# Kernel optimization log

Hardware: AMD Instinct MI355X
Metric: run time of the kernel (lower is better)

Reference implementation:

```python
import jax, jax.numpy as jnp
import numpy as np

H, D, CR, SEL_K = 8, 64, 32, 16          # query heads, head dim, block size, top-k blocks
ROPE_DIM, THETA, WINDOW, GROUPS = 32, 10000.0, 512, 2
INTER, HID, QC = 512, 1024, 256
NEG = -1e30


def _rope_cache(t):
    half = ROPE_DIM // 2
    inv = 1.0 / (THETA ** (jnp.arange(half, dtype=jnp.float32) * 2.0 / ROPE_DIM))
    ang = jnp.arange(t, dtype=jnp.float32)[:, None] * inv[None, :]  # (t, half)
    return jnp.cos(ang), jnp.sin(ang)


def _apply_partial_rope(x, cos, sin):
    half = ROPE_DIM // 2
    x1, x2, rest = x[..., :half], x[..., half:ROPE_DIM], x[..., ROPE_DIM:]
    return jnp.concatenate([x1 * cos - x2 * sin, x1 * sin + x2 * cos, rest], -1)


def _rmsnorm(x, g, eps=1e-6):
    return x * jax.lax.rsqrt(jnp.mean(x * x, -1, keepdims=True) + eps) * g


def setup_inputs():
    key = jax.random.key(0)
    ks = jax.random.split(key, 9)
    f = lambda k, shp, s: jax.random.normal(k, shp, jnp.float32) * s
    return {
        "h": f(ks[0], (1, 2048, HID), 1.0),
        "w_qc": f(ks[1], (HID, QC), QC ** -0.5),
        "w_qup": f(ks[2], (QC, H * D), (H * D) ** -0.5),
        "w_k": f(ks[3], (HID, D), HID ** -0.5),
        "w_v": f(ks[4], (HID, D), HID ** -0.5),
        "g_qnorm": jnp.ones((D,), jnp.float32),
        "g_knorm": jnp.ones((D,), jnp.float32),
        "w_gate": f(ks[5], (D, 3), 0.05),
        "b_gate": jnp.zeros((3,), jnp.float32),
        "sink_logit": f(ks[6], (H,), 0.1),
        "w_out_group": f(ks[7], (GROUPS, (H // GROUPS) * D, INTER), 0.05),
        "w_out": f(ks[8], (GROUPS * INTER, HID), 0.03),
    }


def reference(h, w_qc, w_qup, w_k, w_v, g_qnorm, g_knorm, w_gate, b_gate,
              sink_logit, w_out_group, w_out):
    b, t, _ = h.shape
    cos, sin = _rope_cache(t)
    q = (h @ w_qc @ w_qup).reshape(b, t, H, D).transpose(0, 2, 1, 3)  # (b,H,t,D)
    q = _rmsnorm(_apply_partial_rope(q, cos, sin), g_qnorm)
    k = _rmsnorm(_apply_partial_rope(h @ w_k, cos, sin), g_knorm)      # (b,t,D)
    v = h @ w_v                                                        # (b,t,D)
    scale = 1.0 / np.sqrt(D).astype(np.float32)
    qpos = jnp.arange(t)
    sink = jnp.broadcast_to(sink_logit[None, :, None, None], (b, H, t, 1))

    # ---- compressed branch: attend over block-mean pooled K/V ----
    nb = t // CR
    kc = k[:, :nb * CR].reshape(b, nb, CR, D).mean(2)                  # (b,nb,D)
    vc = v[:, :nb * CR].reshape(b, nb, CR, D).mean(2)
    comp_valid = ((jnp.arange(nb) + 1) * CR - 1)[None, :] <= qpos[:, None]  # (t,nb)
    any_blk = comp_valid.any(-1, keepdims=True)                        # (t,1)
    safe = jnp.where(any_blk, comp_valid, True)
    sc_raw = jnp.einsum('bhqd,bnd->bhqn', q, kc) * scale
    pc = jax.nn.softmax(jnp.concatenate([jnp.where(safe, sc_raw, NEG), sink], -1), -1)
    comp_out = jnp.einsum('bhqn,bnd->bhqd', pc[..., :nb], vc)
    comp_out = jnp.where(any_blk[None, None], comp_out, 0.0)

    # ---- selective branch: top-k blocks per query, dense-masked gather-equivalent ----
    sel_sc = jnp.where(comp_valid, sc_raw, -jnp.inf)
    top_idx = jax.lax.top_k(sel_sc, min(SEL_K, nb))[1]                 # (b,H,t,K)
    sel_blocks = (top_idx[..., :, None] == jnp.arange(nb)).any(-2)     # (b,H,t,nb)
    block_of = jnp.minimum(qpos // CR, nb - 1)
    causal = qpos[:, None] >= qpos[None, :]                            # (t,t)
    in_range = qpos < nb * CR
    tok_sel = sel_blocks[..., block_of] & (causal & in_range[None, :])[None, None]
    scores_full = jnp.einsum('bhqd,bkd->bhqk', q, k) * scale           # (b,H,t,t)
    ps = jax.nn.softmax(jnp.where(tok_sel, scores_full, NEG), -1)
    sel_out = jnp.einsum('bhqk,bkd->bhqd', ps, v)

    # ---- sliding-window branch ----
    sw = causal & ((qpos[:, None] - qpos[None, :]) < WINDOW)
    pw = jax.nn.softmax(
        jnp.concatenate([jnp.where(sw[None, None], scores_full, NEG), sink], -1), -1)
    sw_out = jnp.einsum('bhqk,bkd->bhqd', pw[..., :t], v)

    # ---- learned gate over the three branches ----
    g = jax.nn.sigmoid(q @ w_gate + b_gate)                            # (b,H,t,3)
    g = g / jnp.clip(g.sum(-1, keepdims=True), 1e-6)
    mixed = g[..., 0:1] * comp_out + g[..., 1:2] * sel_out + g[..., 2:3] * sw_out

    # ---- grouped output projection ----
    x = mixed.transpose(0, 2, 1, 3).reshape(b, t, GROUPS, (H // GROUPS) * D)
    y = jnp.einsum('btgf,gfi->btgi', x, w_out_group).reshape(b, t, GROUPS * INTER)
    return y @ w_out
```

## Files before the change

kernel.cpp:

```cpp
#include <hip/hip_runtime.h>
#include <hip/hip_bf16.h>
#include <float.h>
#include <math.h>

typedef __hip_bfloat16 bf16;
typedef float v2f __attribute__((ext_vector_type(2)));

#define NEGBIG (-1e30f)

__device__ __forceinline__ float ldv(const float* p, int i) { return p[i]; }

__device__ __forceinline__ float wave_sum(float v) {
#pragma unroll
  for (int off = 32; off; off >>= 1) v += __shfl_xor(v, off, 64);
  return v;
}
__device__ __forceinline__ float wave_max(float v) {
#pragma unroll
  for (int off = 32; off; off >>= 1) v = fmaxf(v, __shfl_xor(v, off, 64));
  return v;
}

__device__ __forceinline__ float rdlane(float v, int l) {
  return __uint_as_float(__builtin_amdgcn_readlane(__float_as_uint(v), l));
}

template <int L0>
__device__ __forceinline__ void pv16(const float* __restrict__ vp, float e,
                                     float& a0, float& a1, float& a2, float& a3) {
#pragma unroll
  for (int t = 0; t < 16; t += 4) {
    float p0 = rdlane(e, L0 + t + 0);
    float p1 = rdlane(e, L0 + t + 1);
    float p2 = rdlane(e, L0 + t + 2);
    float p3 = rdlane(e, L0 + t + 3);
    a0 += p0 * vp[(t + 0) * 64];
    a1 += p1 * vp[(t + 1) * 64];
    a2 += p2 * vp[(t + 2) * 64];
    a3 += p3 * vp[(t + 3) * 64];
  }
}

__device__ __forceinline__ float qk_dot(const float4* __restrict__ qr,
                                        const float4* __restrict__ kp) {
  v2f d01 = {0.f, 0.f}, d23 = {0.f, 0.f};
#pragma unroll 1
  for (int i = 0; i < 16; i += 2) {
    float4 q0 = qr[i],     k0 = kp[i * 32];
    float4 q1 = qr[i + 1], k1 = kp[i * 32 + 32];
    d01 += (v2f){q0.x, q0.y} * (v2f){k0.x, k0.y};
    d23 += (v2f){q0.z, q0.w} * (v2f){k0.z, k0.w};
    d01 += (v2f){q1.x, q1.y} * (v2f){k1.x, k1.y};
    d23 += (v2f){q1.z, q1.w} * (v2f){k1.z, k1.w};
  }
  v2f d = d01 + d23;
  return d.x + d.y;
}

__device__ __forceinline__ void gemm_core(
    const float* __restrict__ A, const float* __restrict__ B, float* __restrict__ C,
    int K, int lda, int ldb, int ldc, int row0, int col0)
{
  __shared__ __align__(16) float As[2][16][68];
  __shared__ __align__(16) float Bs[2][16][68];
  const int tid = threadIdx.x;
  const int tx = tid & 15, ty = tid >> 4;
  const int ar = tid >> 2;
  const int ak = (tid & 3) * 4;
  const int bk = tid >> 4;
  const int bc = (tid & 15) * 4;

  const int nk = K >> 4;
  float4 a4 = *reinterpret_cast<const float4*>(&A[(row0 + ar) * lda + ak]);
  float4 b4 = *reinterpret_cast<const float4*>(&B[bk * ldb + col0 + bc]);
  {
    As[0][ak + 0][ar] = a4.x; As[0][ak + 1][ar] = a4.y;
    As[0][ak + 2][ar] = a4.z; As[0][ak + 3][ar] = a4.w;
    *reinterpret_cast<float4*>(&Bs[0][bk][bc]) = b4;
  }

  v2f acc01[4] = {};
  v2f acc23[4] = {};
  for (int t = 0; t < nk; ++t) {
    const int cur = t & 1;
    if (t + 1 < nk) {
      int k0 = (t + 1) * 16;
      a4 = *reinterpret_cast<const float4*>(&A[(row0 + ar) * lda + k0 + ak]);
      b4 = *reinterpret_cast<const float4*>(&B[(k0 + bk) * ldb + col0 + bc]);
    }
    __syncthreads();
#pragma unroll
    for (int kk = 0; kk < 16; ++kk) {
      float4 av = *reinterpret_cast<const float4*>(&As[cur][kk][ty * 4]);
      float4 bv = *reinterpret_cast<const float4*>(&Bs[cur][kk][tx * 4]);
      v2f b01; b01.x = bv.x; b01.y = bv.y;
      v2f b23; b23.x = bv.z; b23.y = bv.w;
      float a[4] = {av.x, av.y, av.z, av.w};
#pragma unroll
      for (int i = 0; i < 4; ++i) {
        v2f as; as.x = a[i]; as.y = a[i];
        acc01[i] += as * b01;
        acc23[i] += as * b23;
      }
    }
    if (t + 1 < nk) {
      const int nxt = cur ^ 1;
      As[nxt][ak + 0][ar] = a4.x; As[nxt][ak + 1][ar] = a4.y;
      As[nxt][ak + 2][ar] = a4.z; As[nxt][ak + 3][ar] = a4.w;
      *reinterpret_cast<float4*>(&Bs[nxt][bk][bc]) = b4;
    }
  }
#pragma unroll
  for (int i = 0; i < 4; ++i) {
    float4 o = make_float4(acc01[i].x, acc01[i].y, acc23[i].x, acc23[i].y);
    *reinterpret_cast<float4*>(&C[(row0 + ty * 4 + i) * ldc + col0 + tx * 4]) = o;
  }
}

__global__ __launch_bounds__(256) void gemm_tile(
    const float* __restrict__ A, const float* __restrict__ B, float* __restrict__ C,
    int M, int N, int K, int lda, int ldb, int ldc)
{
  gemm_core(A, B, C, K, lda, ldb, ldc, blockIdx.y * 64, blockIdx.x * 64);
}

__global__ __launch_bounds__(256) void gemm_kv(
    const float* __restrict__ A, const float* __restrict__ B0, const float* __restrict__ B1,
    float* __restrict__ C0, float* __restrict__ C1, int K, int lda, int ldb, int ldc)
{
  const float* B = blockIdx.x ? B1 : B0;
  float* C = blockIdx.x ? C1 : C0;
  gemm_core(A, B, C, K, lda, ldb, ldc, blockIdx.y * 64, 0);
}

__global__ __launch_bounds__(256) void gemm_dual(
    const float* __restrict__ A0, const float* __restrict__ A1,
    const float* __restrict__ B0, const float* __restrict__ B1,
    float* __restrict__ C0, float* __restrict__ C1,
    int K, int lda, int ldb, int ldc, int nx)
{
  const bool second = (int)blockIdx.x >= nx;
  const float* A = second ? A1 : A0;
  const float* B = second ? B1 : B0;
  float* C = second ? C1 : C0;
  const int bx = second ? (blockIdx.x - nx) : blockIdx.x;
  gemm_core(A, B, C, K, lda, ldb, ldc, blockIdx.y * 64, bx * 64);
}

__global__ __launch_bounds__(256) void rope_table_kernel(float* __restrict__ ct,
                                                         float* __restrict__ st) {
  int tid = blockIdx.x * 256 + threadIdx.x;
  if (tid >= 2048 * 16) return;
  int pos = tid >> 4, i = tid & 15;
  double ang = (double)pos * pow(10000.0, -(double)i / 16.0);
  ct[tid] = (float)cos(ang);
  st[tid] = (float)sin(ang);
}

__global__ __launch_bounds__(256) void rope_rms_kernel(
    float* __restrict__ x, const float* __restrict__ g, int rows, int posShift,
    float* __restrict__ kS, const float* __restrict__ ct, const float* __restrict__ st)
{
  const int lane = threadIdx.x & 63;
  const int wid = threadIdx.x >> 6;
  const int r = blockIdx.x * 4 + wid;
  if (r >= rows) return;
  const int pos = r >> posShift;
  float val = x[r * 64 + lane];
  float p = __shfl_xor(val, 16, 64);
  float out = val;
  if (lane < 32) {
    int i = lane & 15;
    float cc = ct[pos * 16 + i], ss = st[pos * 16 + i];
    out = (lane < 16) ? (val * cc - p * ss) : (p * ss + val * cc);
  }
  float ms = wave_sum(out * out) * (1.0f / 64.0f);
  float rn = rsqrtf(ms + 1e-6f);
  float res = out * rn * ldv(g, lane);
  x[r * 64 + lane] = res;
  if (kS) {
    int f4 = (r >> 5) * 512 + (lane >> 2) * 32 + (r & 31);
    kS[f4 * 4 + (lane & 3)] = res;
  }
}

__global__ void compress_kernel(const float* __restrict__ k, const float* __restrict__ v,
                                float* __restrict__ kcT4, float* __restrict__ vc)
{
  const int n = blockIdx.x;
  const int d = threadIdx.x;
  float sk = 0.f, sv = 0.f;
  for (int j = 0; j < 32; ++j) {
    sk += k[(n * 32 + j) * 64 + d];
    sv += v[(n * 32 + j) * 64 + d];
  }
  kcT4[(d >> 2) * 256 + n * 4 + (d & 3)] = sk * (1.0f / 32.0f);
  vc[n * 64 + d] = sv * (1.0f / 32.0f);
}

__global__ __launch_bounds__(256) void attn_kernel(
    const float* __restrict__ q, const float* __restrict__ kS, const float* __restrict__ vbuf,
    const float* __restrict__ kcT4, const float* __restrict__ vc,
    const float* __restrict__ w_gate, const float* __restrict__ b_gate,
    const float* __restrict__ sink, float* __restrict__ mixed)
{
  __shared__ __align__(16) float shq[4][64];
  __shared__ int shsel[4][16];
  const int lane = threadIdx.x & 63;
  const int wid = threadIdx.x >> 6;
  const int bid = 4095 - blockIdx.x;
  const int r = bid * 4 + wid;
  const int qpos = r >> 3, h = r & 7;
  const float scale = 0.125f;

  float qv = q[r * 64 + lane];
  shq[wid][lane] = qv;

  float z0 = qv * ldv(w_gate, lane * 3 + 0);
  float z1 = qv * ldv(w_gate, lane * 3 + 1);
  float z2 = qv * ldv(w_gate, lane * 3 + 2);
  z0 = wave_sum(z0) + ldv(b_gate, 0);
  z1 = wave_sum(z1) + ldv(b_gate, 1);
  z2 = wave_sum(z2) + ldv(b_gate, 2);
  float ga0 = 1.f / (1.f + expf(-z0));
  float ga1 = 1.f / (1.f + expf(-z1));
  float ga2 = 1.f / (1.f + expf(-z2));
  float gs = fmaxf(ga0 + ga1 + ga2, 1e-6f);
  float ginv = 1.f / gs;
  ga0 *= ginv; ga1 *= ginv; ga2 *= ginv;

  const float4* qr = reinterpret_cast<const float4*>(&shq[wid][0]);
  const float4* ks4 = reinterpret_cast<const float4*>(kS);
  const float4* kct = reinterpret_cast<const float4*>(kcT4);
  const float snk = ldv(sink, h);
  const int nv = (qpos + 1) >> 5;

  float sc;
  {
    float d0 = 0.f, d1 = 0.f;
#pragma unroll 1
    for (int i = 0; i < 16; i += 2) {
      float4 q0 = qr[i],     k0 = kct[i * 64 + lane];
      float4 q1 = qr[i + 1], k1 = kct[(i + 1) * 64 + lane];
      d0 += q0.x * k0.x + q0.z * k0.z;
      d1 += q0.y * k0.y + q0.w * k0.w;
      d0 += q1.x * k1.x + q1.z * k1.z;
      d1 += q1.y * k1.y + q1.w * k1.w;
    }
    sc = (d0 + d1) * scale;
  }

  float comp_out = 0.f;
  if (nv > 0) {
    float scomp = (lane < nv) ? sc : NEGBIG;
    float m = fmaxf(wave_max(scomp), snk);
    float e = (lane < nv) ? expf(sc - m) : 0.f;
    float S = wave_sum(e) + expf(snk - m);
    float pn = e / S;
    const float* vcp = vc + lane;
    float c0 = 0.f, c1 = 0.f, c2 = 0.f, c3 = 0.f;
    pv16<0>(vcp, pn, c0, c1, c2, c3);
    pv16<16>(vcp + 1024, pn, c0, c1, c2, c3);
    pv16<32>(vcp + 2048, pn, c0, c1, c2, c3);
    pv16<48>(vcp + 3072, pn, c0, c1, c2, c3);
    comp_out = (c0 + c1) + (c2 + c3);
  }

  {
    float selv = (lane < nv) ? sc : -FLT_MAX;
#pragma unroll
    for (int it = 0; it < 16; ++it) {
      float bv = selv; int bi = lane;
#pragma unroll
      for (int off = 32; off; off >>= 1) {
        float ov = __shfl_xor(bv, off, 64);
        int oi = __shfl_xor(bi, off, 64);
        if (ov > bv || (ov == bv && oi < bi)) { bv = ov; bi = oi; }
      }
      if (lane == 0) shsel[wid][it] = bi;
      if (lane == bi) selv = -INFINITY;
    }
  }

  float M = NEGBIG, S = 0.f, osel = 0.f;
#pragma unroll 1
  for (int c = 0; c < 8; ++c) {
    int b0 = shsel[wid][2 * c], b1 = shsel[wid][2 * c + 1];
    int base0 = b0 * 32, base1 = b1 * 32;
    if (base0 > qpos && base1 > qpos) continue;
    int myb = (lane < 32) ? b0 : b1;
    int tok = myb * 32 + (lane & 31);
    bool ok = (tok <= qpos);
    const float4* kp = ks4 + myb * 512 + (lane & 31);
    float s = ok ? qk_dot(qr, kp) * scale : NEGBIG;
    float Mn = fmaxf(M, wave_max(s));
    float e = ok ? expf(s - Mn) : 0.f;
    float cs = wave_sum(e);
    float corr = expf(M - Mn);
    S = S * corr + cs;
    const float* v0 = vbuf + base0 * 64 + lane;
    const float* v1 = vbuf + base1 * 64 + lane;
    float a0 = 0.f, a1 = 0.f, a2 = 0.f, a3 = 0.f;
    pv16<0>(v0, e, a0, a1, a2, a3);
    pv16<16>(v0 + 1024, e, a0, a1, a2, a3);
    pv16<32>(v1, e, a0, a1, a2, a3);
    pv16<48>(v1 + 1024, e, a0, a1, a2, a3);
    osel = osel * corr + ((a0 + a1) + (a2 + a3));
    M = Mn;
  }
  osel /= S;

  float Mw = NEGBIG, Sw = 0.f, osw = 0.f;
  int kstart = qpos - 511; if (kstart < 0) kstart = 0;
  int sbf = kstart >> 5, sbl = qpos >> 5;
#pragma unroll 1
  for (int sb = sbf; sb <= sbl; sb += 2) {
    int sb1 = sb + 1;
    bool v1ok = (sb1 <= sbl);
    int sb1c = v1ok ? sb1 : sb;
    int myb = (lane < 32) ? sb : sb1c;
    int tok = myb * 32 + (lane & 31);
    bool ok = (tok >= kstart) && (tok <= qpos) && ((lane < 32) || v1ok);
    const float4* kp = ks4 + myb * 512 + (lane & 31);
    float s = ok ? qk_dot(qr, kp) * scale : NEGBIG;
    float Mn = fmaxf(Mw, wave_max(s));
    float e = ok ? expf(s - Mn) : 0.f;
    float cs = wave_sum(e);
    float corr = expf(Mw - Mn);
    Sw = Sw * corr + cs;
    const float* v0 = vbuf + sb * 2048 + lane;
    const float* v1 = vbuf + sb1c * 2048 + lane;
    float a0 = 0.f, a1 = 0.f, a2 = 0.f, a3 = 0.f;
    pv16<0>(v0, e, a0, a1, a2, a3);
    pv16<16>(v0 + 1024, e, a0, a1, a2, a3);
    pv16<32>(v1, e, a0, a1, a2, a3);
    pv16<48>(v1 + 1024, e, a0, a1, a2, a3);
    osw = osw * corr + ((a0 + a1) + (a2 + a3));
    Mw = Mn;
  }
  {
    float Mf = fmaxf(Mw, snk);
    float corr = expf(Mw - Mf);
    float Sf = Sw * corr + expf(snk - Mf);
    osw = osw * corr / Sf;
  }

  mixed[r * 64 + lane] = ga0 * comp_out + ga1 * osel + ga2 * osw;
}

extern "C" void kernel_launch(void* const* d_in, const int* in_sizes, int n_in,
                              void* d_out, int out_size, void* d_ws, size_t ws_size,
                              hipStream_t stream) {
  const float* h      = (const float*)d_in[0];
  const float* w_qc   = (const float*)d_in[1];
  const float* w_qup  = (const float*)d_in[2];
  const float* w_k    = (const float*)d_in[3];
  const float* w_v    = (const float*)d_in[4];
  const float* g_qn   = (const float*)d_in[5];
  const float* g_kn   = (const float*)d_in[6];
  const float* w_gate = (const float*)d_in[7];
  const float* b_gate = (const float*)d_in[8];
  const float* sink   = (const float*)d_in[9];
  const float* wog    = (const float*)d_in[10];
  const float* w_out  = (const float*)d_in[11];
  float* out = (float*)d_out;

  float* ws = (float*)d_ws;
  float* hc  = ws;
  float* qb  = hc + 2048 * 256;
  float* kb  = qb + 2048 * 512;
  float* vb  = kb + 2048 * 64;
  float* vc  = vb + 2048 * 64;
  float* mx  = vc + 64 * 64;
  float* y1  = mx + 2048 * 512;
  float* kS  = y1 + 2048 * 1024;
  float* kct4 = kS + 2048 * 64;
  float* ct  = kct4 + 16 * 64 * 4;
  float* st  = ct + 2048 * 16;

  dim3 blk(256);
  rope_table_kernel<<<dim3(128), blk, 0, stream>>>(ct, st);
  gemm_tile<<<dim3(4, 32), blk, 0, stream>>>(h, w_qc, hc, 2048, 256, 1024, 1024, 256, 256);
  gemm_tile<<<dim3(8, 32), blk, 0, stream>>>(hc, w_qup, qb, 2048, 512, 256, 256, 512, 512);
  gemm_kv<<<dim3(2, 32), blk, 0, stream>>>(h, w_k, w_v, kb, vb, 1024, 1024, 64, 64);
  rope_rms_kernel<<<dim3(4096), blk, 0, stream>>>(qb, g_qn, 16384, 3, nullptr, ct, st);
  rope_rms_kernel<<<dim3(512), blk, 0, stream>>>(kb, g_kn, 2048, 0, kS, ct, st);
  compress_kernel<<<dim3(64), dim3(64), 0, stream>>>(kb, vb, kct4, vc);
  attn_kernel<<<dim3(4096), blk, 0, stream>>>(qb, kS, vb, kct4, vc, w_gate, b_gate, sink, mx);
  gemm_dual<<<dim3(16, 32), blk, 0, stream>>>(mx, mx + 256, wog, wog + 256 * 512,
                                              y1, y1 + 512, 256, 512, 512, 1024, 8);
  gemm_tile<<<dim3(16, 32), blk, 0, stream>>>(y1, w_out, out, 2048, 1024, 1024, 1024, 1024, 1024);
}
```

Baseline: 477.4 us.

## Use 128-thread GEMM blocks with 8x4 microtiles and fuse small launches

The shared GEMM core now runs with 128 threads per 64x64 tile, so each thread computes an 8x4 output microtile and loads two float4s per operand per stage. The aim is more register-level reuse of each shared-memory read. The h@w_qc, h@w_k and h@w_v GEMMs are merged into one launch, and the q and k rope/rmsnorm passes are merged into one launch, which cuts launch overhead and lets the small kernels fill the GPU together. The trade-off is more registers per thread and half as many threads per block, which lowers the number of waves available to hide latency.

After: 499.1 us. +4.5%, slower.

```diff
diff --git a/kernel.cpp b/kernel.cpp
--- a/kernel.cpp
+++ b/kernel.cpp
@@ -65,39 +65,47 @@
   __shared__ __align__(16) float Bs[2][16][68];
   const int tid = threadIdx.x;
   const int tx = tid & 15, ty = tid >> 4;
-  const int ar = tid >> 2;
-  const int ak = (tid & 3) * 4;
-  const int bk = tid >> 4;
-  const int bc = (tid & 15) * 4;
+  const int ar = tid >> 1;
+  const int ak = (tid & 1) * 8;
+  const int bk = tid >> 3;
+  const int bc = (tid & 7) * 8;
 
   const int nk = K >> 4;
-  float4 a4 = *reinterpret_cast<const float4*>(&A[(row0 + ar) * lda + ak]);
-  float4 b4 = *reinterpret_cast<const float4*>(&B[bk * ldb + col0 + bc]);
+  float4 a40 = *reinterpret_cast<const float4*>(&A[(row0 + ar) * lda + ak]);
+  float4 a41 = *reinterpret_cast<const float4*>(&A[(row0 + ar) * lda + ak + 4]);
+  float4 b40 = *reinterpret_cast<const float4*>(&B[bk * ldb + col0 + bc]);
+  float4 b41 = *reinterpret_cast<const float4*>(&B[bk * ldb + col0 + bc + 4]);
   {
-    As[0][ak + 0][ar] = a4.x; As[0][ak + 1][ar] = a4.y;
-    As[0][ak + 2][ar] = a4.z; As[0][ak + 3][ar] = a4.w;
-    *reinterpret_cast<float4*>(&Bs[0][bk][bc]) = b4;
-  }
-
-  v2f acc01[4] = {};
-  v2f acc23[4] = {};
+    As[0][ak + 0][ar] = a40.x; As[0][ak + 1][ar] = a40.y;
+    As[0][ak + 2][ar] = a40.z; As[0][ak + 3][ar] = a40.w;
+    As[0][ak + 4][ar] = a41.x; As[0][ak + 5][ar] = a41.y;
+    As[0][ak + 6][ar] = a41.z; As[0][ak + 7][ar] = a41.w;
+    *reinterpret_cast<float4*>(&Bs[0][bk][bc]) = b40;
+    *reinterpret_cast<float4*>(&Bs[0][bk][bc + 4]) = b41;
+  }
+
+  v2f acc01[8] = {};
+  v2f acc23[8] = {};
   for (int t = 0; t < nk; ++t) {
     const int cur = t & 1;
     if (t + 1 < nk) {
       int k0 = (t + 1) * 16;
-      a4 = *reinterpret_cast<const float4*>(&A[(row0 + ar) * lda + k0 + ak]);
-      b4 = *reinterpret_cast<const float4*>(&B[(k0 + bk) * ldb + col0 + bc]);
+      a40 = *reinterpret_cast<const float4*>(&A[(row0 + ar) * lda + k0 + ak]);
+      a41 = *reinterpret_cast<const float4*>(&A[(row0 + ar) * lda + k0 + ak + 4]);
+      b40 = *reinterpret_cast<const float4*>(&B[(k0 + bk) * ldb + col0 + bc]);
+      b41 = *reinterpret_cast<const float4*>(&B[(k0 + bk) * ldb + col0 + bc + 4]);
     }
     __syncthreads();
 #pragma unroll
     for (int kk = 0; kk < 16; ++kk) {
-      float4 av = *reinterpret_cast<const float4*>(&As[cur][kk][ty * 4]);
-      float4 bv = *reinterpret_cast<const float4*>(&Bs[cur][kk][tx * 4]);
+      float4 av0 = *reinterpret_cast<const float4*>(&As[cur][kk][ty * 8]);
+      float4 av1 = *reinterpret_cast<const float4*>(&As[cur][kk][ty * 8 + 4]);
+      float4 bv  = *reinterpret_cast<const float4*>(&Bs[cur][kk][tx * 4]);
       v2f b01; b01.x = bv.x; b01.y = bv.y;
       v2f b23; b23.x = bv.z; b23.y = bv.w;
-      float a[4] = {av.x, av.y, av.z, av.w};
-#pragma unroll
-      for (int i = 0; i < 4; ++i) {
+      float a[8] = {av0.x, av0.y, av0.z, av0.w, av1.x, av1.y, av1.z, av1.w};
+#pragma unroll
+      for (int i = 0; i < 8; ++i) {
         v2f as; as.x = a[i]; as.y = a[i];
         acc01[i] += as * b01;
         acc23[i] += as * b23;
@@ -105,35 +113,44 @@
     }
     if (t + 1 < nk) {
       const int nxt = cur ^ 1;
-      As[nxt][ak + 0][ar] = a4.x; As[nxt][ak + 1][ar] = a4.y;
-      As[nxt][ak + 2][ar] = a4.z; As[nxt][ak + 3][ar] = a4.w;
-      *reinterpret_cast<float4*>(&Bs[nxt][bk][bc]) = b4;
+      As[nxt][ak + 0][ar] = a40.x; As[nxt][ak + 1][ar] = a40.y;
+      As[nxt][ak + 2][ar] = a40.z; As[nxt][ak + 3][ar] = a40.w;
+      As[nxt][ak + 4][ar] = a41.x; As[nxt][ak + 5][ar] = a41.y;
+      As[nxt][ak + 6][ar] = a41.z; As[nxt][ak + 7][ar] = a41.w;
+      *reinterpret_cast<float4*>(&Bs[nxt][bk][bc]) = b40;
+      *reinterpret_cast<float4*>(&Bs[nxt][bk][bc + 4]) = b41;
     }
   }
 #pragma unroll
-  for (int i = 0; i < 4; ++i) {
+  for (int i = 0; i < 8; ++i) {
     float4 o = make_float4(acc01[i].x, acc01[i].y, acc23[i].x, acc23[i].y);
-    *reinterpret_cast<float4*>(&C[(row0 + ty * 4 + i) * ldc + col0 + tx * 4]) = o;
-  }
-}
-
-__global__ __launch_bounds__(256) void gemm_tile(
+    *reinterpret_cast<float4*>(&C[(row0 + ty * 8 + i) * ldc + col0 + tx * 4]) = o;
+  }
+}
+
+__global__ __launch_bounds__(128) void gemm_tile(
     const float* __restrict__ A, const float* __restrict__ B, float* __restrict__ C,
     int M, int N, int K, int lda, int ldb, int ldc)
 {
   gemm_core(A, B, C, K, lda, ldb, ldc, blockIdx.y * 64, blockIdx.x * 64);
 }
 
-__global__ __launch_bounds__(256) void gemm_kv(
-    const float* __restrict__ A, const float* __restrict__ B0, const float* __restrict__ B1,
-    float* __restrict__ C0, float* __restrict__ C1, int K, int lda, int ldb, int ldc)
-{
-  const float* B = blockIdx.x ? B1 : B0;
-  float* C = blockIdx.x ? C1 : C0;
-  gemm_core(A, B, C, K, lda, ldb, ldc, blockIdx.y * 64, 0);
-}
-
-__global__ __launch_bounds__(256) void gemm_dual(
+__global__ __launch_bounds__(128) void gemm_qckv(
+    const float* __restrict__ h, const float* __restrict__ w_qc,
+    const float* __restrict__ w_k, const float* __restrict__ w_v,
+    float* __restrict__ hc, float* __restrict__ kb, float* __restrict__ vb)
+{
+  const int x = blockIdx.x;
+  if (x < 4) {
+    gemm_core(h, w_qc, hc, 1024, 1024, 256, 256, blockIdx.y * 64, x * 64);
+  } else if (x == 4) {
+    gemm_core(h, w_k, kb, 1024, 1024, 64, 64, blockIdx.y * 64, 0);
+  } else {
+    gemm_core(h, w_v, vb, 1024, 1024, 64, 64, blockIdx.y * 64, 0);
+  }
+}
+
+__global__ __launch_bounds__(128) void gemm_dual(
     const float* __restrict__ A0, const float* __restrict__ A1,
     const float* __restrict__ B0, const float* __restrict__ B1,
     float* __restrict__ C0, float* __restrict__ C1,
@@ -157,13 +174,14 @@
   st[tid] = (float)sin(ang);
 }
 
-__global__ __launch_bounds__(256) void rope_rms_kernel(
+__device__ __forceinline__ void rope_body(
     float* __restrict__ x, const float* __restrict__ g, int rows, int posShift,
-    float* __restrict__ kS, const float* __restrict__ ct, const float* __restrict__ st)
+    float* __restrict__ kS, const float* __restrict__ ct, const float* __restrict__ st,
+    int bx)
 {
   const int lane = threadIdx.x & 63;
   const int wid = threadIdx.x >> 6;
-  const int r = blockIdx.x * 4 + wid;
+  const int r = bx * 4 + wid;
   if (r >= rows) return;
   const int pos = r >> posShift;
   float val = x[r * 64 + lane];
@@ -182,6 +200,16 @@
     int f4 = (r >> 5) * 512 + (lane >> 2) * 32 + (r & 31);
     kS[f4 * 4 + (lane & 3)] = res;
   }
+}
+
+__global__ __launch_bounds__(256) void rope_rms_fused(
+    float* __restrict__ qx, float* __restrict__ kx,
+    const float* __restrict__ gq, const float* __restrict__ gk,
+    float* __restrict__ kS, const float* __restrict__ ct, const float* __restrict__ st)
+{
+  const int bx = blockIdx.x;
+  if (bx < 4096) rope_body(qx, gq, 16384, 3, nullptr, ct, st, bx);
+  else           rope_body(kx, gk, 2048, 0, kS, ct, st, bx - 4096);
 }
 
 __global__ void compress_kernel(const float* __restrict__ k, const float* __restrict__ v,
@@ -379,15 +407,14 @@
   float* st  = ct + 2048 * 16;
 
   dim3 blk(256);
+  dim3 blk128(128);
   rope_table_kernel<<<dim3(128), blk, 0, stream>>>(ct, st);
-  gemm_tile<<<dim3(4, 32), blk, 0, stream>>>(h, w_qc, hc, 2048, 256, 1024, 1024, 256, 256);
-  gemm_tile<<<dim3(8, 32), blk, 0, stream>>>(hc, w_qup, qb, 2048, 512, 256, 256, 512, 512);
-  gemm_kv<<<dim3(2, 32), blk, 0, stream>>>(h, w_k, w_v, kb, vb, 1024, 1024, 64, 64);
-  rope_rms_kernel<<<dim3(4096), blk, 0, stream>>>(qb, g_qn, 16384, 3, nullptr, ct, st);
-  rope_rms_kernel<<<dim3(512), blk, 0, stream>>>(kb, g_kn, 2048, 0, kS, ct, st);
+  gemm_qckv<<<dim3(6, 32), blk128, 0, stream>>>(h, w_qc, w_k, w_v, hc, kb, vb);
+  gemm_tile<<<dim3(8, 32), blk128, 0, stream>>>(hc, w_qup, qb, 2048, 512, 256, 256, 512, 512);
+  rope_rms_fused<<<dim3(4608), blk, 0, stream>>>(qb, kb, g_qn, g_kn, kS, ct, st);
   compress_kernel<<<dim3(64), dim3(64), 0, stream>>>(kb, vb, kct4, vc);
   attn_kernel<<<dim3(4096), blk, 0, stream>>>(qb, kS, vb, kct4, vc, w_gate, b_gate, sink, mx);
-  gemm_dual<<<dim3(16, 32), blk, 0, stream>>>(mx, mx + 256, wog, wog + 256 * 512,
-                                              y1, y1 + 512, 256, 512, 512, 1024, 8);
-  gemm_tile<<<dim3(16, 32), blk, 0, stream>>>(y1, w_out, out, 2048, 1024, 1024, 1024, 1024, 1024);
-}
+  gemm_dual<<<dim3(16, 32), blk128, 0, stream>>>(mx, mx + 256, wog, wog + 256 * 512,
+                                                 y1, y1 + 512, 256, 512, 512, 1024, 8);
+  gemm_tile<<<dim3(16, 32), blk128, 0, stream>>>(y1, w_out, out, 2048, 1024, 1024, 1024, 1024, 1024);
+}
```
